# Optimization experiments

Measured on AMD Instinct MI355X. Metric: run time of the kernel, lower is better.

## Reference

```python
import jax, jax.numpy as jnp
import numpy as np

D_MODEL = 2048
NUM_HEADS = 16
HEAD_DIM = D_MODEL // NUM_HEADS
B, S = 2, 2048


def rotate_half(x):
    x1, x2 = jnp.split(x, 2, axis=-1)
    return jnp.concatenate((-x2, x1), axis=-1)


def setup_inputs() -> dict:
    key = jax.random.key(0)
    ks = jax.random.split(key, 7)
    x = jax.random.normal(ks[0], (B, S, D_MODEL), dtype=jnp.float32)
    cos = jax.random.normal(ks[1], (1, 1, S, HEAD_DIM), dtype=jnp.float32)
    sin = jax.random.normal(ks[2], (1, 1, S, HEAD_DIM), dtype=jnp.float32)
    scale = 1.0 / np.sqrt(D_MODEL)
    Wq = jax.random.normal(ks[3], (D_MODEL, D_MODEL), dtype=jnp.float32) * scale
    Wk = jax.random.normal(ks[4], (D_MODEL, D_MODEL), dtype=jnp.float32) * scale
    Wv = jax.random.normal(ks[5], (D_MODEL, D_MODEL), dtype=jnp.float32) * scale
    Wo = jax.random.normal(ks[6], (D_MODEL, D_MODEL), dtype=jnp.float32) * scale
    return {"x": x, "cos": cos, "sin": sin, "Wq": Wq, "Wk": Wk, "Wv": Wv, "Wo": Wo}


def reference(x, cos, sin, Wq, Wk, Wv, Wo):
    Bb, Ss, Dd = x.shape
    H, hd = NUM_HEADS, HEAD_DIM
    # nn.Linear: y = x @ W.T ; here W stored as [out, in]
    q = (x @ Wq.T).reshape(Bb, Ss, H, hd).transpose(0, 2, 1, 3)  # [B,H,S,hd]
    k = (x @ Wk.T).reshape(Bb, Ss, H, hd).transpose(0, 2, 1, 3)
    v = (x @ Wv.T).reshape(Bb, Ss, H, hd).transpose(0, 2, 1, 3)
    q = q * cos + rotate_half(q) * sin
    k = k * cos + rotate_half(k) * sin
    scale = 1.0 / jnp.sqrt(jnp.asarray(hd, dtype=x.dtype))
    scores = jnp.einsum('bhqd,bhkd->bhqk', q, k) * scale  # [B,H,S,S]
    causal = jnp.tril(jnp.ones((Ss, Ss), dtype=bool))
    scores = jnp.where(causal[None, None], scores, jnp.finfo(x.dtype).min)
    attn = jax.nn.softmax(scores, axis=-1)
    out = jnp.einsum('bhqk,bhkd->bhqd', attn, v)  # [B,H,S,hd]
    out = out.transpose(0, 2, 1, 3).reshape(Bb, Ss, Dd)
    return out @ Wo.T
```

## Files before the change

kernel.cpp:

```cpp
#include <hip/hip_runtime.h>

typedef unsigned short u16;
typedef __attribute__((ext_vector_type(8))) short bf8v;
typedef __attribute__((ext_vector_type(4))) float f4v;

#define DEV static __device__ __forceinline__

DEV float bf2f(u16 u){ unsigned x = ((unsigned)u) << 16; float f; __builtin_memcpy(&f, &x, 4); return f; }
DEV u16 f2bf(float f){ unsigned x; __builtin_memcpy(&x, &f, 4); x += 0x7fff + ((x >> 16) & 1); return (u16)(x >> 16); }

DEV void async16(const void* g, void* l){
  __builtin_amdgcn_global_load_lds((const __attribute__((address_space(1))) unsigned*)g,
                                   (__attribute__((address_space(3))) unsigned*)l, 16, 0, 0);
}

DEV void vwait6(){ asm volatile("s_waitcnt vmcnt(6)" ::: "memory"); }
DEV void vwait0(){ asm volatile("s_waitcnt vmcnt(0)" ::: "memory"); }
DEV void bar(){ asm volatile("s_barrier" ::: "memory"); }

__global__ __launch_bounds__(256) void f2b_k(const float* __restrict__ src,
                                             u16* __restrict__ dst)
{
  const long i = ((long)blockIdx.x * 256 + threadIdx.x) * 4;
  const float4 v = *(const float4*)(src + i);
  ushort4 o;
  o.x = f2bf(v.x); o.y = f2bf(v.y); o.z = f2bf(v.z); o.w = f2bf(v.w);
  *(ushort4*)(dst + i) = o;
}

__global__ __launch_bounds__(256) void f2b3_k(const float* __restrict__ a,
                                              const float* __restrict__ b,
                                              const float* __restrict__ c,
                                              u16* __restrict__ dst)
{
  const int bx = blockIdx.x;
  const float* s = bx < 4096 ? a : (bx < 8192 ? b : c);
  const long soff = ((long)(bx & 4095) * 256 + threadIdx.x) * 4;
  const long doff = ((long)bx * 256 + threadIdx.x) * 4;
  const float4 v = *(const float4*)(s + soff);
  ushort4 o;
  o.x = f2bf(v.x); o.y = f2bf(v.y); o.z = f2bf(v.z); o.w = f2bf(v.w);
  *(ushort4*)(dst + doff) = o;
}

constexpr int KDIM = 2048;

__global__ __launch_bounds__(512, 2) void gemm256(const u16* __restrict__ A,
                                                  const u16* __restrict__ B,
                                                  u16* __restrict__ C0,
                                                  u16* __restrict__ C1,
                                                  u16* __restrict__ C2,
                                                  float* __restrict__ Cf, int mode)
{
  __shared__ __align__(16) u16 Asm[3][8192];
  __shared__ __align__(16) u16 Bsm[3][16384];

  const int tid = threadIdx.x;
  const int w = tid >> 6, lane = tid & 63;
  const int ln = lane & 15, quad = lane >> 4;
  const int wr = w >> 2, wc = w & 3;

  const int gx = gridDim.x;
  const int nwg = gx * gridDim.y;
  const int wg = blockIdx.y * gx + blockIdx.x;
  const int swz = (wg & 7) * (nwg >> 3) + (wg >> 3);
  const int bx = swz % gx, by = swz / gx;
  const long m0 = (long)by << 7, n0 = (long)bx << 8;

  f4v acc[4][4] = {};

  const int colb = (w & 1) * 32 + quad * 8;
  const int wh = w >> 1;
  long gRow[4];
#pragma unroll
  for (int r = 0; r < 4; ++r) gRow[r] = (long)((r * 4 + wh) * 16 + ln) * KDIM;
  const u16* gA = A + m0 * KDIM + colb;
  const u16* gB = B + n0 * KDIM + colb;

#define STA(sl, r, kt) async16(gA + gRow[r] + (kt), (char*)Asm + (sl)*16384 + (r)*8192 + w*1024)
#define STB(sl, r, kt) async16(gB + gRow[r] + (kt), (char*)Bsm + (sl)*32768 + (r)*8192 + w*1024)

  STA(0,0,0);  STA(0,1,0);  STB(0,0,0);  STB(0,1,0);  STB(0,2,0);  STB(0,3,0);
  STA(1,0,64); STA(1,1,64); STB(1,0,64); STB(1,1,64); STB(1,2,64); STB(1,3,64);
  vwait6();
  bar();

  int sA = 0, sB = 1, sC = 2;
  const int nt = KDIM / 64;
  for (int t = 0; t < nt; ++t) {
    const u16* Ab = Asm[sA];
    const u16* Bb = Bsm[sA];
    const long kn = (long)(t + 2) * 64;
    const bool st = (t + 2 < nt);
    bf8v a[4][2], bl[2][2], bh[2][2];

#pragma unroll
    for (int i = 0; i < 4; ++i)
#pragma unroll
      for (int ks = 0; ks < 2; ++ks)
        a[i][ks] = *(const bf8v*)&Ab[(((wr * 4 + i) * 2 + ks) * 64 + lane) * 8];
#pragma unroll
    for (int j = 0; j < 2; ++j)
#pragma unroll
      for (int ks = 0; ks < 2; ++ks)
        bl[j][ks] = *(const bf8v*)&Bb[(((wc * 4 + j) * 2 + ks) * 64 + lane) * 8];
    if (st) { STA(sC, 0, kn); STA(sC, 1, kn); STB(sC, 0, kn); }
    bar();
    __builtin_amdgcn_s_setprio(1);
#pragma unroll
    for (int ks = 0; ks < 2; ++ks)
#pragma unroll
      for (int i = 0; i < 4; ++i)
#pragma unroll
        for (int j = 0; j < 2; ++j)
          acc[i][j] = __builtin_amdgcn_mfma_f32_16x16x32_bf16(a[i][ks], bl[j][ks], acc[i][j], 0, 0, 0);
    __builtin_amdgcn_s_setprio(0);

#pragma unroll
    for (int j = 0; j < 2; ++j)
#pragma unroll
      for (int ks = 0; ks < 2; ++ks)
        bh[j][ks] = *(const bf8v*)&Bb[(((wc * 4 + 2 + j) * 2 + ks) * 64 + lane) * 8];
    if (st) { STB(sC, 1, kn); STB(sC, 2, kn); STB(sC, 3, kn); }
    if (t < nt - 2) vwait6(); else vwait0();
    bar();
    __builtin_amdgcn_s_setprio(1);
#pragma unroll
    for (int ks = 0; ks < 2; ++ks)
#pragma unroll
      for (int i = 0; i < 4; ++i)
#pragma unroll
        for (int j = 0; j < 2; ++j)
          acc[i][2 + j] = __builtin_amdgcn_mfma_f32_16x16x32_bf16(a[i][ks], bh[j][ks], acc[i][2 + j], 0, 0, 0);
    __builtin_amdgcn_s_setprio(0);

    const int tmp = sA; sA = sB; sB = sC; sC = tmp;
  }
#undef STA
#undef STB

#pragma unroll
  for (int i = 0; i < 4; i++) {
    const long mrow = m0 + wr * 64 + i * 16 + quad * 4;
#pragma unroll
    for (int j = 0; j < 4; j++) {
      const long ncol = n0 + wc * 64 + j * 16 + ln;
#pragma unroll
      for (int r = 0; r < 4; r++) {
        const float fv = acc[i][j][r];
        const long m = mrow + r;
        if (mode == 0) {
          C0[m * 2048 + ncol] = f2bf(fv);
        } else if (mode == 2) {
          Cf[m * 2048 + ncol] = fv;
        } else if (mode == 1) {
          const long s = m & 2047, bb = m >> 11;
          const long hh = ncol >> 7, dc = ncol & 127;
          C0[((bb * 16 + hh) * 128 + dc) * 2048 + s] = f2bf(fv);
        } else {
          const int sec = (int)(n0 >> 11);
          const long nc = ncol & 2047;
          if (sec == 0)      C0[m * 2048 + nc] = f2bf(fv);
          else if (sec == 1) C1[m * 2048 + nc] = f2bf(fv);
          else {
            const long s = m & 2047, bb = m >> 11;
            const long hh = nc >> 7, dc = nc & 127;
            C2[((bb * 16 + hh) * 128 + dc) * 2048 + s] = f2bf(fv);
          }
        }
      }
    }
  }
}

__global__ __launch_bounds__(256) void rope2_k(u16* __restrict__ qb,
                                               u16* __restrict__ kb,
                                               const float* __restrict__ cs,
                                               const float* __restrict__ sn)
{
  const long idx = (long)blockIdx.x * 256 + threadIdx.x;
  u16* t = (idx >= 4194304) ? kb : qb;
  const long i2 = idx & 4194303;
  const long m = i2 >> 10;
  const int rest = (int)(i2 & 1023);
  const int h = rest >> 6, d = rest & 63;
  const int s = (int)(m & 2047);
  const long base = m * 2048 + h * 128 + d;
  const float a  = bf2f(t[base]), b = bf2f(t[base + 64]);
  const float c1 = cs[s * 128 + d],      s1 = sn[s * 128 + d];
  const float c2 = cs[s * 128 + d + 64], s2 = sn[s * 128 + d + 64];
  t[base]      = f2bf(a * c1 - b * s1);
  t[base + 64] = f2bf(b * c2 + a * s2);
}

__global__ __launch_bounds__(256) void attn_k(const u16* __restrict__ q,
                                              const u16* __restrict__ k,
                                              const u16* __restrict__ vt,
                                              u16* __restrict__ ao)
{
  __shared__ __align__(16) u16 Ks[128 * 128];
  __shared__ __align__(16) u16 Vs[128 * 128];
  __shared__ __align__(16) u16 Ps[4 * 16 * 72];
  const int qt = 31 - blockIdx.x;
  const int bh = blockIdx.y;
  const int b = bh >> 4, h = bh & 15;
  const int tid = threadIdx.x;
  const int w = tid >> 6, lane = tid & 63;
  const int ln = lane & 15, quad = lane >> 4;
  const int q0 = qt << 6;

  const u16* kb0 = k + ((long)(b * 2048 + (tid & 15))) * 2048 + h * 128
                     + ((tid >> 6) & 3) * 32 + ((tid >> 4) & 3) * 8;
  const u16* vb0 = vt + ((long)(bh * 128 + (tid & 15))) * 2048
                      + ((tid >> 6) & 1) * 32 + ((tid >> 4) & 3) * 8;
  const int tb = tid >> 7;

  bf8v aq[4];
  {
    const u16* qp = q + ((long)(b * 2048 + q0 + w * 16 + ln)) * 2048 + h * 128;
#pragma unroll
    for (int dt = 0; dt < 4; ++dt) aq[dt] = *(const bf8v*)(qp + dt * 32 + quad * 8);
  }
  f4v O[8] = {};
  f4v Osum = {};
  const short one_bf = (short)0x3F80;
  const bf8v vones = {one_bf, one_bf, one_bf, one_bf, one_bf, one_bf, one_bf, one_bf};

  const int nktp = qt >> 1;
  for (int ktp = 0; ktp <= nktp; ++ktp) {
    const int k0s = ktp << 7;
    const bool has1 = (2 * ktp + 1) <= qt;

    __syncthreads();
#pragma unroll
    for (int it = 0; it < 8; ++it) {
      const int rowu = (it >> 2) * 64 + (it & 3) * 16;
      async16(kb0 + (long)(k0s + rowu) * 2048, (char*)Ks + it * 4096 + w * 1024);
    }
#pragma unroll
    for (int it = 0; it < 8; ++it) {
      const int g = 2 * it + tb;
      const long off = (long)((g & 7) * 16) * 2048 + (g >> 3) * 64 + k0s;
      async16(vb0 + off, (char*)Vs + it * 4096 + w * 1024);
    }
    __syncthreads();

    f4v S[8];
#pragma unroll
    for (int jt = 0; jt < 8; jt++) {
      if (jt >= 4 && !has1) { S[jt] = (f4v){-1e30f, -1e30f, -1e30f, -1e30f}; continue; }
      const int sub = jt >> 2, jl = jt & 3;
      f4v s = {};
#pragma unroll
      for (int dt = 0; dt < 4; dt++) {
        const bf8v bk = *(const bf8v*)&Ks[(sub * 1024 + (jl * 4 + dt) * 64 + lane) * 8];
        s = __builtin_amdgcn_mfma_f32_16x16x32_bf16(aq[dt], bk, s, 0, 0, 0);
      }
      S[jt] = s;
    }
    const float scl = 0.08838834764831845f;
    const float shift = 20.0f;
    if (ktp == nktp) {
      const int qi_loc = w * 16 + quad * 4;
#pragma unroll
      for (int jt = 0; jt < 8; jt++) {
        const int dcol = k0s - q0 + (jt >> 2) * 64 + (jt & 3) * 16 + ln;
#pragma unroll
        for (int r = 0; r < 4; r++) {
          const float arg = (dcol > qi_loc + r) ? -1e30f : (S[jt][r] * scl - shift);
          S[jt][r] = __expf(arg);
        }
      }
    } else {
#pragma unroll
      for (int jt = 0; jt < 8; jt++)
#pragma unroll
        for (int r = 0; r < 4; r++) S[jt][r] = __expf(S[jt][r] * scl - shift);
    }
    const int wbase = w * 16 * 72;
#pragma unroll
    for (int sub = 0; sub < 2; ++sub) {
      if (sub == 1 && !has1) break;
#pragma unroll
      for (int jl = 0; jl < 4; jl++)
#pragma unroll
        for (int r = 0; r < 4; r++)
          Ps[wbase + (quad * 4 + r) * 72 + jl * 16 + ln] = f2bf(S[sub * 4 + jl][r]);
      bf8v ap[2];
#pragma unroll
      for (int k2 = 0; k2 < 2; k2++)
        ap[k2] = *(const bf8v*)&Ps[wbase + ln * 72 + k2 * 32 + quad * 8];
#pragma unroll
      for (int nt = 0; nt < 8; nt++) {
#pragma unroll
        for (int k2 = 0; k2 < 2; k2++) {
          const bf8v bv = *(const bf8v*)&Vs[(sub * 1024 + (nt * 2 + k2) * 64 + lane) * 8];
          O[nt] = __builtin_amdgcn_mfma_f32_16x16x32_bf16(ap[k2], bv, O[nt], 0, 0, 0);
        }
      }
#pragma unroll
      for (int k2 = 0; k2 < 2; k2++)
        Osum = __builtin_amdgcn_mfma_f32_16x16x32_bf16(ap[k2], vones, Osum, 0, 0, 0);
    }
  }

  float inv[4];
#pragma unroll
  for (int r = 0; r < 4; r++) inv[r] = 1.0f / Osum[r];
  const long ob = ((long)(b * 2048 + q0 + w * 16 + quad * 4)) * 2048 + h * 128 + ln;
#pragma unroll
  for (int r = 0; r < 4; r++)
#pragma unroll
    for (int nt = 0; nt < 8; nt++)
      ao[ob + (long)r * 2048 + nt * 16] = f2bf(O[nt][r] * inv[r]);
}

extern "C" void kernel_launch(void* const* d_in, const int* in_sizes, int n_in,
                              void* d_out, int out_size, void* d_ws, size_t ws_size,
                              hipStream_t stream) {
  const float* x  = (const float*)d_in[0];
  const float* cs = (const float*)d_in[1];
  const float* sn = (const float*)d_in[2];
  const float* Wq = (const float*)d_in[3];
  const float* Wk = (const float*)d_in[4];
  const float* Wv = (const float*)d_in[5];
  const float* Wo = (const float*)d_in[6];
  float* out = (float*)d_out;

  const size_t E = 4194304;
  u16* xb = (u16*)d_ws;

  const size_t need = 11 * E * sizeof(u16);
  if (ws_size >= need) {
    u16* wqkv = xb + 2 * E;
    u16* qb   = wqkv + 3 * E;
    u16* kb   = qb + 2 * E;
    u16* vtb  = kb + 2 * E;
    u16* aob  = xb;

    f2b_k<<<8192, 256, 0, stream>>>(x, xb);
    f2b3_k<<<12288, 256, 0, stream>>>(Wq, Wk, Wv, wqkv);
    gemm256<<<dim3(24, 32), 512, 0, stream>>>(xb, wqkv, qb, kb, vtb, nullptr, 3);
    rope2_k<<<32768, 256, 0, stream>>>(qb, kb, cs, sn);
    attn_k<<<dim3(32, 32), 256, 0, stream>>>(qb, kb, vtb, aob);
    f2b_k<<<4096, 256, 0, stream>>>(Wo, wqkv);
    gemm256<<<dim3(8, 32), 512, 0, stream>>>(aob, wqkv, nullptr, nullptr, nullptr, out, 2);
  } else {
    u16* wb  = xb + 2 * E;
    u16* qb  = wb + E;
    u16* kb  = qb + 2 * E;
    u16* vtb = kb + 2 * E;
    u16* aob = xb;

    f2b_k<<<8192, 256, 0, stream>>>(x, xb);
    f2b_k<<<4096, 256, 0, stream>>>(Wq, wb);
    gemm256<<<dim3(8, 32), 512, 0, stream>>>(xb, wb, qb, nullptr, nullptr, nullptr, 0);
    f2b_k<<<4096, 256, 0, stream>>>(Wk, wb);
    gemm256<<<dim3(8, 32), 512, 0, stream>>>(xb, wb, kb, nullptr, nullptr, nullptr, 0);
    f2b_k<<<4096, 256, 0, stream>>>(Wv, wb);
    gemm256<<<dim3(8, 32), 512, 0, stream>>>(xb, wb, vtb, nullptr, nullptr, nullptr, 1);
    rope2_k<<<32768, 256, 0, stream>>>(qb, kb, cs, sn);
    attn_k<<<dim3(32, 32), 256, 0, stream>>>(qb, kb, vtb, aob);
    f2b_k<<<4096, 256, 0, stream>>>(Wo, wb);
    gemm256<<<dim3(8, 32), 512, 0, stream>>>(aob, wb, nullptr, nullptr, nullptr, out, 2);
  }
}
```

Baseline: 530.6 us.

## Restructure GEMM LDS staging by k-half instead of by N-half

Changes the global-to-LDS load layout so each thread loads one row segment per k-subtile (one for A, two for B), and splits each 64-wide k tile into two 32-wide halves. Each half now runs a full 4x4 MFMA block, where before the block was split by N into two 4x2 blocks over the full k. The intent is simpler addressing, fewer live fragment registers, and a more even interleave of async loads with compute. It adds two extra barriers per iteration, and the new LDS layout may change bank conflicts.

```diff
diff --git a/kernel.cpp b/kernel.cpp
--- a/kernel.cpp
+++ b/kernel.cpp
@@ -69,75 +69,67 @@
 
   f4v acc[4][4] = {};
 
-  const int colb = (w & 1) * 32 + quad * 8;
-  const int wh = w >> 1;
-  long gRow[4];
-#pragma unroll
-  for (int r = 0; r < 4; ++r) gRow[r] = (long)((r * 4 + wh) * 16 + ln) * KDIM;
-  const u16* gA = A + m0 * KDIM + colb;
-  const u16* gB = B + n0 * KDIM + colb;
-
-#define STA(sl, r, kt) async16(gA + gRow[r] + (kt), (char*)Asm + (sl)*16384 + (r)*8192 + w*1024)
-#define STB(sl, r, kt) async16(gB + gRow[r] + (kt), (char*)Bsm + (sl)*32768 + (r)*8192 + w*1024)
-
-  STA(0,0,0);  STA(0,1,0);  STB(0,0,0);  STB(0,1,0);  STB(0,2,0);  STB(0,3,0);
-  STA(1,0,64); STA(1,1,64); STB(1,0,64); STB(1,1,64); STB(1,2,64); STB(1,3,64);
+  const u16* pA  = A + (m0 + w * 16 + ln) * (long)KDIM + quad * 8;
+  const u16* pB0 = B + (n0 + w * 16 + ln) * (long)KDIM + quad * 8;
+  const u16* pB1 = B + (n0 + (8 + w) * 16 + ln) * (long)KDIM + quad * 8;
+  char* ldsA = (char*)Asm + (long)tid * 16;
+  char* ldsB = (char*)Bsm + (long)tid * 16;
+
+#define STG(sl, ks, kt) do{                                                     \
+    async16(pA  + (kt) + (ks) * 32, ldsA + (sl) * 16384 + (ks) * 8192);         \
+    async16(pB0 + (kt) + (ks) * 32, ldsB + (sl) * 32768 + (ks) * 16384);        \
+    async16(pB1 + (kt) + (ks) * 32, ldsB + (sl) * 32768 + (ks) * 16384 + 8192); \
+  }while(0)
+
+  STG(0, 0, 0);  STG(0, 1, 0);
+  STG(1, 0, 64); STG(1, 1, 64);
   vwait6();
   bar();
 
-  int sA = 0, sB = 1, sC = 2;
+  int s0 = 0, s1 = 1, s2 = 2;
   const int nt = KDIM / 64;
   for (int t = 0; t < nt; ++t) {
-    const u16* Ab = Asm[sA];
-    const u16* Bb = Bsm[sA];
-    const long kn = (long)(t + 2) * 64;
+    const u16* Ab = Asm[s0];
+    const u16* Bb = Bsm[s0];
     const bool st = (t + 2 < nt);
-    bf8v a[4][2], bl[2][2], bh[2][2];
-
-#pragma unroll
-    for (int i = 0; i < 4; ++i)
-#pragma unroll
-      for (int ks = 0; ks < 2; ++ks)
-        a[i][ks] = *(const bf8v*)&Ab[(((wr * 4 + i) * 2 + ks) * 64 + lane) * 8];
-#pragma unroll
-    for (int j = 0; j < 2; ++j)
-#pragma unroll
-      for (int ks = 0; ks < 2; ++ks)
-        bl[j][ks] = *(const bf8v*)&Bb[(((wc * 4 + j) * 2 + ks) * 64 + lane) * 8];
-    if (st) { STA(sC, 0, kn); STA(sC, 1, kn); STB(sC, 0, kn); }
+    const long kt2 = (long)(t + 2) * 64;
+
+    bf8v a0[4], b0[4];
+#pragma unroll
+    for (int i = 0; i < 4; ++i) a0[i] = *(const bf8v*)&Ab[((wr * 4 + i) * 64 + lane) * 8];
+#pragma unroll
+    for (int j = 0; j < 4; ++j) b0[j] = *(const bf8v*)&Bb[((wc * 4 + j) * 64 + lane) * 8];
+    if (st) STG(s2, 0, kt2);
     bar();
     __builtin_amdgcn_s_setprio(1);
 #pragma unroll
-    for (int ks = 0; ks < 2; ++ks)
-#pragma unroll
-      for (int i = 0; i < 4; ++i)
-#pragma unroll
-        for (int j = 0; j < 2; ++j)
-          acc[i][j] = __builtin_amdgcn_mfma_f32_16x16x32_bf16(a[i][ks], bl[j][ks], acc[i][j], 0, 0, 0);
+    for (int i = 0; i < 4; ++i)
+#pragma unroll
+      for (int j = 0; j < 4; ++j)
+        acc[i][j] = __builtin_amdgcn_mfma_f32_16x16x32_bf16(a0[i], b0[j], acc[i][j], 0, 0, 0);
     __builtin_amdgcn_s_setprio(0);
-
-#pragma unroll
-    for (int j = 0; j < 2; ++j)
-#pragma unroll
-      for (int ks = 0; ks < 2; ++ks)
-        bh[j][ks] = *(const bf8v*)&Bb[(((wc * 4 + 2 + j) * 2 + ks) * 64 + lane) * 8];
-    if (st) { STB(sC, 1, kn); STB(sC, 2, kn); STB(sC, 3, kn); }
-    if (t < nt - 2) vwait6(); else vwait0();
+    bar();
+
+    bf8v a1[4], b1[4];
+#pragma unroll
+    for (int i = 0; i < 4; ++i) a1[i] = *(const bf8v*)&Ab[((8 + wr * 4 + i) * 64 + lane) * 8];
+#pragma unroll
+    for (int j = 0; j < 4; ++j) b1[j] = *(const bf8v*)&Bb[((16 + wc * 4 + j) * 64 + lane) * 8];
+    if (st) STG(s2, 1, kt2);
+    if (st) vwait6(); else vwait0();
     bar();
     __builtin_amdgcn_s_setprio(1);
 #pragma unroll
-    for (int ks = 0; ks < 2; ++ks)
-#pragma unroll
-      for (int i = 0; i < 4; ++i)
-#pragma unroll
-        for (int j = 0; j < 2; ++j)
-          acc[i][2 + j] = __builtin_amdgcn_mfma_f32_16x16x32_bf16(a[i][ks], bh[j][ks], acc[i][2 + j], 0, 0, 0);
+    for (int i = 0; i < 4; ++i)
+#pragma unroll
+      for (int j = 0; j < 4; ++j)
+        acc[i][j] = __builtin_amdgcn_mfma_f32_16x16x32_bf16(a1[i], b1[j], acc[i][j], 0, 0, 0);
     __builtin_amdgcn_s_setprio(0);
-
-    const int tmp = sA; sA = sB; sB = sC; sC = tmp;
-  }
-#undef STA
-#undef STB
+    bar();
+
+    const int tmp = s0; s0 = s1; s1 = s2; s2 = tmp;
+  }
+#undef STG
 
 #pragma unroll
   for (int i = 0; i < 4; i++) {
```

Result: no change. 534.0 us (+0.7%).
